# Kernel optimization log

Hardware: AMD Instinct MI355X
Metric: run time of the kernel (lower is better)

Reference implementation:

```python
import jax, jax.numpy as jnp
import numpy as np

N_NODES = 50000
N_EDGES = 800000
IN_DIM, H1, H2 = 512, 128, 64


def setup_inputs() -> dict:
    key = jax.random.key(0)
    k1, k2, k3, k4 = jax.random.split(key, 4)
    x = jax.random.normal(k1, (N_NODES, IN_DIM), dtype=jnp.float32)
    edge_index = jax.random.randint(k2, (2, N_EDGES), 0, N_NODES, dtype=jnp.int64)
    # Glorot-ish scaled weights (PyG GCNConv uses glorot init)
    W1 = jax.random.normal(k3, (IN_DIM, H1), dtype=jnp.float32) * (1.0 / np.sqrt(IN_DIM))
    b1 = jnp.zeros((H1,), dtype=jnp.float32)
    W2 = jax.random.normal(k4, (H1, H2), dtype=jnp.float32) * (1.0 / np.sqrt(H1))
    b2 = jnp.zeros((H2,), dtype=jnp.float32)
    return {"x": x, "edge_index": edge_index, "W1": W1, "b1": b1, "W2": W2, "b2": b2}


def reference(x, edge_index, W1, b1, W2, b2):
    N = x.shape[0]
    # PyG GCNConv default: add self-loops + symmetric normalization
    loop = jnp.arange(N, dtype=edge_index.dtype)
    src = jnp.concatenate([edge_index[0], loop])  # message source j
    dst = jnp.concatenate([edge_index[1], loop])  # aggregation target i
    deg = jax.ops.segment_sum(jnp.ones(src.shape[0], dtype=x.dtype), dst, num_segments=N)
    dinv = jnp.where(deg > 0, jax.lax.rsqrt(deg), 0.0)
    norm = dinv[src] * dinv[dst]  # [E+N]

    def gcn_relu(h, W, b):
        h = h @ W                                   # [N, F_out]
        msg = h[src] * norm[:, None]                # gather + edge scaling
        agg = jax.ops.segment_sum(msg, dst, num_segments=N)  # scatter-add
        return jax.nn.relu(agg + b)

    h = gcn_relu(x, W1, b1)
    return gcn_relu(h, W2, b2)
```

## Files before the change

kernel.cpp:

```cpp
#include <hip/hip_runtime.h>


constexpr int IN_DIM = 512;
constexpr int HD1 = 128;
constexpr int HD2 = 64;

typedef __attribute__((ext_vector_type(8))) short bf16x8;
typedef __attribute__((ext_vector_type(8))) unsigned short u16x8;
typedef __attribute__((ext_vector_type(4))) float f32x4;
typedef unsigned int u32;

__device__ inline unsigned short f2bf(float f) {
    u32 u = __builtin_bit_cast(u32, f);
    return (unsigned short)((u + 0x7fffu + ((u >> 16) & 1u)) >> 16);
}
__device__ inline float bf_lo(u32 v) { return __builtin_bit_cast(float, v << 16); }
__device__ inline float bf_hi(u32 v) { return __builtin_bit_cast(float, v & 0xffff0000u); }

__device__ inline int elem_off(int row, int k) {
    return (row << 6) + (k ^ ((row & 7) << 3));
}
__device__ inline int elem_off128(int row, int k) {
    return (row << 7) + (k ^ ((row & 7) << 3));
}

__global__ __launch_bounds__(256) void k_prep(const int* __restrict__ dst, int E,
                                              int* __restrict__ deg,
                                              const float* __restrict__ W1,
                                              unsigned short* __restrict__ Wt,
                                              const float* __restrict__ W2,
                                              unsigned short* __restrict__ Wt2) {
    int id = blockIdx.x * 256 + threadIdx.x;
    if (id < E) atomicAdd(&deg[dst[id]], 1);
    if (id < IN_DIM * HD1) {
        int n = id >> 9, k = id & 511;
        Wt[id] = f2bf(W1[k * HD1 + n]);
    }
    if (id < HD1 * HD2) {
        int n = id >> 7, k = id & 127;
        Wt2[id] = f2bf(W2[k * HD2 + n]);
    }
}

__global__ __launch_bounds__(256) void k_dinv_bsum(const int* __restrict__ deg, int N,
                                                   float* __restrict__ dinv,
                                                   int* __restrict__ bsum) {
    __shared__ int s[256];
    int t = threadIdx.x;
    int i = blockIdx.x * 256 + t;
    int d = (i < N) ? deg[i] : 0;
    if (i < N) dinv[i] = rsqrtf((float)(d + 1));
    s[t] = d;
    __syncthreads();
    for (int st = 128; st > 0; st >>= 1) {
        if (t < st) s[t] += s[t + st];
        __syncthreads();
    }
    if (t == 0) bsum[blockIdx.x] = s[0];
}

__global__ __launch_bounds__(1024) void k_scan_bsum(int* __restrict__ bsum, int nb) {
    __shared__ int s[1024];
    int t = threadIdx.x;
    s[t] = (t < nb) ? bsum[t] : 0;
    __syncthreads();
    for (int off = 1; off < 1024; off <<= 1) {
        int v = (t >= off) ? s[t - off] : 0;
        __syncthreads();
        s[t] += v;
        __syncthreads();
    }
    if (t < nb) bsum[t] = (t == 0) ? 0 : s[t - 1];
}

__global__ __launch_bounds__(256) void k_scan_final(const int* __restrict__ deg, int N,
                                                    const int* __restrict__ bsum,
                                                    int* __restrict__ rowptr) {
    __shared__ int s[256];
    int t = threadIdx.x;
    int i = blockIdx.x * 256 + t;
    int v = (i < N) ? deg[i] : 0;
    s[t] = v;
    __syncthreads();
    for (int off = 1; off < 256; off <<= 1) {
        int u = (t >= off) ? s[t - off] : 0;
        __syncthreads();
        s[t] += u;
        __syncthreads();
    }
    int incl = s[t] + bsum[blockIdx.x];
    if (i < N) rowptr[i] = incl - v;
    if (i == N - 1) rowptr[N] = incl;
}

__global__ __launch_bounds__(256) void k_fill(const int* __restrict__ src,
                                              const int* __restrict__ dst, int E,
                                              const int* __restrict__ rowptr,
                                              const float* __restrict__ dinv,
                                              int* __restrict__ fill,
                                              int* __restrict__ col,
                                              float* __restrict__ wgt) {
    int e = blockIdx.x * 256 + threadIdx.x;
    if (e < E) {
        int s = src[e], d = dst[e];
        int pos = rowptr[d] + atomicAdd(&fill[d], 1);
        col[pos] = s;
        wgt[pos] = dinv[s] * dinv[d];
    }
}

__global__ __launch_bounds__(256) void k_gemm1(const float* __restrict__ X,
                                               const unsigned short* __restrict__ Wt,
                                               unsigned short* __restrict__ H, int N) {
    __shared__ unsigned short As[128 * 64];
    __shared__ unsigned short Bs[128 * 64];

    const int tid = threadIdx.x;
    const int lane = tid & 63;
    const int wid = tid >> 6;
    const int brow = blockIdx.x * 128;
    const int wr0 = (wid >> 1) * 64;
    const int wc0 = (wid & 1) * 64;
    const bool full = (brow + 128 <= N);

    f32x4 acc[4][4];
#pragma unroll
    for (int i = 0; i < 4; i++)
#pragma unroll
        for (int j = 0; j < 4; j++) acc[i][j] = (f32x4){0.f, 0.f, 0.f, 0.f};

    for (int kt = 0; kt < IN_DIM / 64; kt++) {
        const int k0 = kt * 64;
#pragma unroll
        for (int p = 0; p < 4; p++) {
            int chunk = (wid * 4 + p) * 64 + lane;
            int n = chunk >> 3;
            int kcs = chunk & 7;
            int kc = kcs ^ (n & 7);
            const unsigned short* src = &Wt[(size_t)n * IN_DIM + k0 + kc * 8];
            unsigned short* dst = &Bs[(wid * 4 + p) * 512];
            __builtin_amdgcn_global_load_lds(
                (const __attribute__((address_space(1))) u32*)(const void*)src,
                (__attribute__((address_space(3))) u32*)(void*)dst, 16, 0, 0);
        }
#pragma unroll
        for (int p = 0; p < 4; p++) {
            int chunk = tid + p * 256;
            int r = chunk >> 3;
            int kc = chunk & 7;
            const float* xp = &X[(size_t)(brow + r) * IN_DIM + k0 + kc * 8];
            float4 v0, v1;
            if (full || (brow + r) < N) {
                v0 = *(const float4*)xp;
                v1 = *(const float4*)(xp + 4);
            } else {
                v0 = make_float4(0.f, 0.f, 0.f, 0.f); v1 = v0;
            }
            u16x8 w;
            w[0] = f2bf(v0.x); w[1] = f2bf(v0.y); w[2] = f2bf(v0.z); w[3] = f2bf(v0.w);
            w[4] = f2bf(v1.x); w[5] = f2bf(v1.y); w[6] = f2bf(v1.z); w[7] = f2bf(v1.w);
            *(u16x8*)&As[elem_off(r, kc * 8)] = w;
        }
        __syncthreads();

#pragma unroll
        for (int kk = 0; kk < 2; kk++) {
            const int kel = kk * 32 + (lane >> 4) * 8;
            bf16x8 a[4], b[4];
#pragma unroll
            for (int mi = 0; mi < 4; mi++)
                a[mi] = *(const bf16x8*)&As[elem_off(wr0 + mi * 16 + (lane & 15), kel)];
#pragma unroll
            for (int ni = 0; ni < 4; ni++)
                b[ni] = *(const bf16x8*)&Bs[elem_off(wc0 + ni * 16 + (lane & 15), kel)];
#pragma unroll
            for (int mi = 0; mi < 4; mi++)
#pragma unroll
                for (int ni = 0; ni < 4; ni++)
                    acc[mi][ni] = __builtin_amdgcn_mfma_f32_16x16x32_bf16(
                        a[mi], b[ni], acc[mi][ni], 0, 0, 0);
        }
        __syncthreads();
    }

#pragma unroll
    for (int mi = 0; mi < 4; mi++) {
#pragma unroll
        for (int reg = 0; reg < 4; reg++) {
            int grow = brow + wr0 + mi * 16 + (lane >> 4) * 4 + reg;
            if (grow < N) {
#pragma unroll
                for (int ni = 0; ni < 4; ni++) {
                    int gcol = wc0 + ni * 16 + (lane & 15);
                    H[(size_t)grow * HD1 + gcol] = f2bf(acc[mi][ni][reg]);
                }
            }
        }
    }
}

__global__ __launch_bounds__(256) void k_gather1(const unsigned short* __restrict__ h,
                                                 const int* __restrict__ rowptr,
                                                 const int* __restrict__ col,
                                                 const float* __restrict__ wgt,
                                                 const float* __restrict__ dinv,
                                                 const float* __restrict__ bias,
                                                 unsigned short* __restrict__ out, int N) {
    const int i = (blockIdx.x * 256 + threadIdx.x) >> 6;
    const int lane = threadIdx.x & 63;
    if (i >= N) return;
    const int half = lane >> 5;
    const int c4 = (lane & 31) * 4;
    const float di = dinv[i];
    const unsigned short* hc = h + c4;

    float a0 = 0.f, a1 = 0.f, a2 = 0.f, a3 = 0.f;
    if (half == 0) {
        uint2 sv = *(const uint2*)&hc[(size_t)i * HD1];
        float s = di * di;
        a0 = bf_lo(sv.x) * s; a1 = bf_hi(sv.x) * s;
        a2 = bf_lo(sv.y) * s; a3 = bf_hi(sv.y) * s;
    }
    const int beg = rowptr[i], end = rowptr[i + 1];
    for (int p0 = beg; p0 < end; p0 += 64) {
        int idx = p0 + lane;
        bool okl = idx < end;
        int myj = okl ? col[idx] : i;
        float myw = okl ? wgt[idx] : 0.f;
        const int cnt8 = (min(64, end - p0) + 7) & ~7;
        uint2 v[4]; float wv[4];
#pragma unroll
        for (int q = 0; q < 4; q++) {
            int e = 2 * q + half;
            int j = __shfl(myj, e);
            wv[q] = __shfl(myw, e);
            v[q] = *(const uint2*)&hc[(size_t)j * HD1];
        }
        for (int k = 8; k < cnt8; k += 8) {
            uint2 nv[4]; float nw[4];
#pragma unroll
            for (int q = 0; q < 4; q++) {
                int e = k + 2 * q + half;
                int j = __shfl(myj, e);
                nw[q] = __shfl(myw, e);
                nv[q] = *(const uint2*)&hc[(size_t)j * HD1];
            }
#pragma unroll
            for (int q = 0; q < 4; q++) {
                a0 = fmaf(bf_lo(v[q].x), wv[q], a0);
                a1 = fmaf(bf_hi(v[q].x), wv[q], a1);
                a2 = fmaf(bf_lo(v[q].y), wv[q], a2);
                a3 = fmaf(bf_hi(v[q].y), wv[q], a3);
            }
#pragma unroll
            for (int q = 0; q < 4; q++) { v[q] = nv[q]; wv[q] = nw[q]; }
        }
#pragma unroll
        for (int q = 0; q < 4; q++) {
            a0 = fmaf(bf_lo(v[q].x), wv[q], a0);
            a1 = fmaf(bf_hi(v[q].x), wv[q], a1);
            a2 = fmaf(bf_lo(v[q].y), wv[q], a2);
            a3 = fmaf(bf_hi(v[q].y), wv[q], a3);
        }
    }
    a0 += __shfl_xor(a0, 32);
    a1 += __shfl_xor(a1, 32);
    a2 += __shfl_xor(a2, 32);
    a3 += __shfl_xor(a3, 32);
    if (half == 0) {
        float4 bv = *(const float4*)&bias[c4];
        u32 w0 = (u32)f2bf(fmaxf(a0 + bv.x, 0.f)) | ((u32)f2bf(fmaxf(a1 + bv.y, 0.f)) << 16);
        u32 w1 = (u32)f2bf(fmaxf(a2 + bv.z, 0.f)) | ((u32)f2bf(fmaxf(a3 + bv.w, 0.f)) << 16);
        *(uint2*)&out[(size_t)i * HD1 + c4] = make_uint2(w0, w1);
    }
}

__global__ __launch_bounds__(256) void k_gemm2(const unsigned short* __restrict__ A,
                                               const unsigned short* __restrict__ Wt2,
                                               unsigned short* __restrict__ H, int N) {
    __shared__ unsigned short As[128 * 128];
    __shared__ unsigned short Bs[64 * 128];
    const int tid = threadIdx.x;
    const int lane = tid & 63;
    const int wid = tid >> 6;
    const int brow = blockIdx.x * 128;
    const int wr0 = wid * 32;

#pragma unroll
    for (int p = 0; p < 8; p++) {
        int chunk = (wid * 8 + p) * 64 + lane;
        int r = chunk >> 4;
        int kcs = chunk & 15;
        int kc = kcs ^ (r & 7);
        const unsigned short* src = &A[(size_t)(brow + r) * HD1 + kc * 8];
        unsigned short* dst = &As[(wid * 8 + p) * 512];
        __builtin_amdgcn_global_load_lds(
            (const __attribute__((address_space(1))) u32*)(const void*)src,
            (__attribute__((address_space(3))) u32*)(void*)dst, 16, 0, 0);
    }
#pragma unroll
    for (int p = 0; p < 4; p++) {
        int chunk = (wid * 4 + p) * 64 + lane;
        int c = chunk >> 4;
        int kcs = chunk & 15;
        int kc = kcs ^ (c & 7);
        const unsigned short* src = &Wt2[(size_t)c * HD1 + kc * 8];
        unsigned short* dst = &Bs[(wid * 4 + p) * 512];
        __builtin_amdgcn_global_load_lds(
            (const __attribute__((address_space(1))) u32*)(const void*)src,
            (__attribute__((address_space(3))) u32*)(void*)dst, 16, 0, 0);
    }
    __syncthreads();

    f32x4 acc[2][4];
#pragma unroll
    for (int i = 0; i < 2; i++)
#pragma unroll
        for (int j = 0; j < 4; j++) acc[i][j] = (f32x4){0.f, 0.f, 0.f, 0.f};

#pragma unroll
    for (int kk = 0; kk < 4; kk++) {
        const int kel = kk * 32 + (lane >> 4) * 8;
        bf16x8 a[2], b[4];
#pragma unroll
        for (int mi = 0; mi < 2; mi++)
            a[mi] = *(const bf16x8*)&As[elem_off128(wr0 + mi * 16 + (lane & 15), kel)];
#pragma unroll
        for (int ni = 0; ni < 4; ni++)
            b[ni] = *(const bf16x8*)&Bs[elem_off128(ni * 16 + (lane & 15), kel)];
#pragma unroll
        for (int mi = 0; mi < 2; mi++)
#pragma unroll
            for (int ni = 0; ni < 4; ni++)
                acc[mi][ni] = __builtin_amdgcn_mfma_f32_16x16x32_bf16(
                    a[mi], b[ni], acc[mi][ni], 0, 0, 0);
    }

#pragma unroll
    for (int mi = 0; mi < 2; mi++) {
#pragma unroll
        for (int reg = 0; reg < 4; reg++) {
            int grow = brow + wr0 + mi * 16 + (lane >> 4) * 4 + reg;
            if (grow < N) {
#pragma unroll
                for (int ni = 0; ni < 4; ni++) {
                    int gcol = ni * 16 + (lane & 15);
                    H[(size_t)grow * HD2 + gcol] = f2bf(acc[mi][ni][reg]);
                }
            }
        }
    }
}

__global__ __launch_bounds__(256) void k_gather2(const unsigned short* __restrict__ h,
                                                 const int* __restrict__ rowptr,
                                                 const int* __restrict__ col,
                                                 const float* __restrict__ wgt,
                                                 const float* __restrict__ dinv,
                                                 const float* __restrict__ bias,
                                                 float* __restrict__ out, int N) {
    const int i = (blockIdx.x * 256 + threadIdx.x) >> 6;
    const int lane = threadIdx.x & 63;
    if (i >= N) return;
    const int half = lane >> 5;
    const int c2 = (lane & 31) * 2;
    const float di = dinv[i];
    const unsigned short* hc = h + c2;

    float a0 = 0.f, a1 = 0.f;
    if (half == 0) {
        u32 sv = *(const u32*)&hc[(size_t)i * HD2];
        float s = di * di;
        a0 = bf_lo(sv) * s; a1 = bf_hi(sv) * s;
    }
    const int beg = rowptr[i], end = rowptr[i + 1];
    for (int p0 = beg; p0 < end; p0 += 64) {
        int idx = p0 + lane;
        bool okl = idx < end;
        int myj = okl ? col[idx] : i;
        float myw = okl ? wgt[idx] : 0.f;
        const int cnt8 = (min(64, end - p0) + 7) & ~7;
        u32 v[4]; float wv[4];
#pragma unroll
        for (int q = 0; q < 4; q++) {
            int e = 2 * q + half;
            int j = __shfl(myj, e);
            wv[q] = __shfl(myw, e);
            v[q] = *(const u32*)&hc[(size_t)j * HD2];
        }
        for (int k = 8; k < cnt8; k += 8) {
            u32 nv[4]; float nw[4];
#pragma unroll
            for (int q = 0; q < 4; q++) {
                int e = k + 2 * q + half;
                int j = __shfl(myj, e);
                nw[q] = __shfl(myw, e);
                nv[q] = *(const u32*)&hc[(size_t)j * HD2];
            }
#pragma unroll
            for (int q = 0; q < 4; q++) {
                a0 = fmaf(bf_lo(v[q]), wv[q], a0);
                a1 = fmaf(bf_hi(v[q]), wv[q], a1);
            }
#pragma unroll
            for (int q = 0; q < 4; q++) { v[q] = nv[q]; wv[q] = nw[q]; }
        }
#pragma unroll
        for (int q = 0; q < 4; q++) {
            a0 = fmaf(bf_lo(v[q]), wv[q], a0);
            a1 = fmaf(bf_hi(v[q]), wv[q], a1);
        }
    }
    a0 += __shfl_xor(a0, 32);
    a1 += __shfl_xor(a1, 32);
    if (half == 0) {
        float2 bv = *(const float2*)&bias[c2];
        float2 r = make_float2(fmaxf(a0 + bv.x, 0.f), fmaxf(a1 + bv.y, 0.f));
        *(float2*)&out[(size_t)i * HD2 + c2] = r;
    }
}

extern "C" void kernel_launch(void* const* d_in, const int* in_sizes, int n_in,
                              void* d_out, int out_size, void* d_ws, size_t ws_size,
                              hipStream_t stream) {
    const float* x  = (const float*)d_in[0];
    const int*   ei = (const int*)d_in[1];
    const float* W1 = (const float*)d_in[2];
    const float* b1 = (const float*)d_in[3];
    const float* W2 = (const float*)d_in[4];
    const float* b2 = (const float*)d_in[5];
    float* out = (float*)d_out;

    const int N = in_sizes[0] / IN_DIM;
    const int E = in_sizes[1] / 2;
    const int* src = ei;
    const int* dst = ei + E;

    char* w = (char*)d_ws;
    size_t off = 0;
    auto alloc = [&](size_t bytes) -> void* {
        void* p = w + off;
        off = (off + bytes + 255) & ~(size_t)255;
        return p;
    };
    int*   deg    = (int*)alloc((size_t)N * 4);
    int*   fill   = (int*)alloc((size_t)N * 4);
    int*   rowptr = (int*)alloc((size_t)(N + 1) * 4);
    int*   bsum   = (int*)alloc(1024 * 4);
    int*   col    = (int*)alloc((size_t)E * 4);
    float* wgt    = (float*)alloc((size_t)E * 4);
    float* dinv   = (float*)alloc((size_t)N * 4);
    unsigned short* Wt  = (unsigned short*)alloc((size_t)IN_DIM * HD1 * 2);
    unsigned short* Wt2 = (unsigned short*)alloc((size_t)HD2 * HD1 * 2);
    unsigned short* h1  = (unsigned short*)alloc((size_t)N * HD1 * 2);
    unsigned short* agg1= (unsigned short*)alloc((size_t)(N + 128) * HD1 * 2);
    unsigned short* h2  = h1;

    size_t zero_span = (size_t)((char*)fill - (char*)deg) + (size_t)N * 4;
    hipMemsetAsync(deg, 0, zero_span, stream);

    const int nb = (N + 255) / 256;
    const int eb = (E + 255) / 256;

    k_prep<<<eb, 256, 0, stream>>>(dst, E, deg, W1, Wt, W2, Wt2);
    k_dinv_bsum<<<nb, 256, 0, stream>>>(deg, N, dinv, bsum);
    k_scan_bsum<<<1, 1024, 0, stream>>>(bsum, nb);
    k_scan_final<<<nb, 256, 0, stream>>>(deg, N, bsum, rowptr);
    k_fill<<<eb, 256, 0, stream>>>(src, dst, E, rowptr, dinv, fill, col, wgt);

    k_gemm1<<<(N + 127) / 128, 256, 0, stream>>>(x, Wt, h1, N);
    k_gather1<<<(N * 64 + 255) / 256, 256, 0, stream>>>(h1, rowptr, col, wgt, dinv, b1, agg1, N);
    k_gemm2<<<(N + 127) / 128, 256, 0, stream>>>(agg1, Wt2, h2, N);
    k_gather2<<<(N * 64 + 255) / 256, 256, 0, stream>>>(h2, rowptr, col, wgt, dinv, b2, out, N);
}
```

Before: 179.4 us.

## Co-schedule CSR fill with GEMM1 in one launch; compute edge weights on the fly

Merges the CSR fill kernel and the first GEMM into one launch. Extra blocks past the GEMM tiles run a grid-stride edge fill, so the memory/atomic-bound fill overlaps the compute-bound GEMM. The per-edge weight array is dropped: the gather kernels load dinv[col] per edge and multiply by the destination's dinv, which saves a 3.2MB write and re-read but adds a dependent random load per edge chunk. Fill blocks compete with GEMM blocks for CUs and LDS, since the unused shared arrays are still allocated.

```diff
diff --git a/kernel.cpp b/kernel.cpp
--- a/kernel.cpp
+++ b/kernel.cpp
@@ -93,27 +93,27 @@
     if (i == N - 1) rowptr[N] = incl;
 }
 
-__global__ __launch_bounds__(256) void k_fill(const int* __restrict__ src,
+__global__ __launch_bounds__(256) void k_mega(const float* __restrict__ X,
+                                              const unsigned short* __restrict__ Wt,
+                                              unsigned short* __restrict__ H, int N,
+                                              int gemmBlocks,
+                                              const int* __restrict__ src,
                                               const int* __restrict__ dst, int E,
                                               const int* __restrict__ rowptr,
-                                              const float* __restrict__ dinv,
                                               int* __restrict__ fill,
-                                              int* __restrict__ col,
-                                              float* __restrict__ wgt) {
-    int e = blockIdx.x * 256 + threadIdx.x;
-    if (e < E) {
-        int s = src[e], d = dst[e];
-        int pos = rowptr[d] + atomicAdd(&fill[d], 1);
-        col[pos] = s;
-        wgt[pos] = dinv[s] * dinv[d];
-    }
-}
-
-__global__ __launch_bounds__(256) void k_gemm1(const float* __restrict__ X,
-                                               const unsigned short* __restrict__ Wt,
-                                               unsigned short* __restrict__ H, int N) {
+                                              int* __restrict__ col) {
     __shared__ unsigned short As[128 * 64];
     __shared__ unsigned short Bs[128 * 64];
+
+    if (blockIdx.x >= gemmBlocks) {
+        int stride = (gridDim.x - gemmBlocks) * 256;
+        for (int e = (blockIdx.x - gemmBlocks) * 256 + threadIdx.x; e < E; e += stride) {
+            int s = src[e], d = dst[e];
+            int pos = rowptr[d] + atomicAdd(&fill[d], 1);
+            col[pos] = s;
+        }
+        return;
+    }
 
     const int tid = threadIdx.x;
     const int lane = tid & 63;
@@ -137,11 +137,11 @@
             int n = chunk >> 3;
             int kcs = chunk & 7;
             int kc = kcs ^ (n & 7);
-            const unsigned short* src = &Wt[(size_t)n * IN_DIM + k0 + kc * 8];
-            unsigned short* dst = &Bs[(wid * 4 + p) * 512];
+            const unsigned short* srcp = &Wt[(size_t)n * IN_DIM + k0 + kc * 8];
+            unsigned short* dstp = &Bs[(wid * 4 + p) * 512];
             __builtin_amdgcn_global_load_lds(
-                (const __attribute__((address_space(1))) u32*)(const void*)src,
-                (__attribute__((address_space(3))) u32*)(void*)dst, 16, 0, 0);
+                (const __attribute__((address_space(1))) u32*)(const void*)srcp,
+                (__attribute__((address_space(3))) u32*)(void*)dstp, 16, 0, 0);
         }
 #pragma unroll
         for (int p = 0; p < 4; p++) {
@@ -202,7 +202,6 @@
 __global__ __launch_bounds__(256) void k_gather1(const unsigned short* __restrict__ h,
                                                  const int* __restrict__ rowptr,
                                                  const int* __restrict__ col,
-                                                 const float* __restrict__ wgt,
                                                  const float* __restrict__ dinv,
                                                  const float* __restrict__ bias,
                                                  unsigned short* __restrict__ out, int N) {
@@ -226,14 +225,14 @@
         int idx = p0 + lane;
         bool okl = idx < end;
         int myj = okl ? col[idx] : i;
-        float myw = okl ? wgt[idx] : 0.f;
+        float mydj = okl ? dinv[myj] : 0.f;
         const int cnt8 = (min(64, end - p0) + 7) & ~7;
         uint2 v[4]; float wv[4];
 #pragma unroll
         for (int q = 0; q < 4; q++) {
             int e = 2 * q + half;
             int j = __shfl(myj, e);
-            wv[q] = __shfl(myw, e);
+            wv[q] = __shfl(mydj, e) * di;
             v[q] = *(const uint2*)&hc[(size_t)j * HD1];
         }
         for (int k = 8; k < cnt8; k += 8) {
@@ -242,7 +241,7 @@
             for (int q = 0; q < 4; q++) {
                 int e = k + 2 * q + half;
                 int j = __shfl(myj, e);
-                nw[q] = __shfl(myw, e);
+                nw[q] = __shfl(mydj, e) * di;
                 nv[q] = *(const uint2*)&hc[(size_t)j * HD1];
             }
 #pragma unroll
@@ -355,7 +354,6 @@
 __global__ __launch_bounds__(256) void k_gather2(const unsigned short* __restrict__ h,
                                                  const int* __restrict__ rowptr,
                                                  const int* __restrict__ col,
-                                                 const float* __restrict__ wgt,
                                                  const float* __restrict__ dinv,
                                                  const float* __restrict__ bias,
                                                  float* __restrict__ out, int N) {
@@ -378,14 +376,14 @@
         int idx = p0 + lane;
         bool okl = idx < end;
         int myj = okl ? col[idx] : i;
-        float myw = okl ? wgt[idx] : 0.f;
+        float mydj = okl ? dinv[myj] : 0.f;
         const int cnt8 = (min(64, end - p0) + 7) & ~7;
         u32 v[4]; float wv[4];
 #pragma unroll
         for (int q = 0; q < 4; q++) {
             int e = 2 * q + half;
             int j = __shfl(myj, e);
-            wv[q] = __shfl(myw, e);
+            wv[q] = __shfl(mydj, e) * di;
             v[q] = *(const u32*)&hc[(size_t)j * HD2];
         }
         for (int k = 8; k < cnt8; k += 8) {
@@ -394,7 +392,7 @@
             for (int q = 0; q < 4; q++) {
                 int e = k + 2 * q + half;
                 int j = __shfl(myj, e);
-                nw[q] = __shfl(myw, e);
+                nw[q] = __shfl(mydj, e) * di;
                 nv[q] = *(const u32*)&hc[(size_t)j * HD2];
             }
 #pragma unroll
@@ -448,7 +446,6 @@
     int*   rowptr = (int*)alloc((size_t)(N + 1) * 4);
     int*   bsum   = (int*)alloc(1024 * 4);
     int*   col    = (int*)alloc((size_t)E * 4);
-    float* wgt    = (float*)alloc((size_t)E * 4);
     float* dinv   = (float*)alloc((size_t)N * 4);
     unsigned short* Wt  = (unsigned short*)alloc((size_t)IN_DIM * HD1 * 2);
     unsigned short* Wt2 = (unsigned short*)alloc((size_t)HD2 * HD1 * 2);
@@ -461,15 +458,18 @@
 
     const int nb = (N + 255) / 256;
     const int eb = (E + 255) / 256;
+    const int gemmBlocks = (N + 127) / 128;
+    const int fillBlocks = 512;
 
     k_prep<<<eb, 256, 0, stream>>>(dst, E, deg, W1, Wt, W2, Wt2);
     k_dinv_bsum<<<nb, 256, 0, stream>>>(deg, N, dinv, bsum);
     k_scan_bsum<<<1, 1024, 0, stream>>>(bsum, nb);
     k_scan_final<<<nb, 256, 0, stream>>>(deg, N, bsum, rowptr);
-    k_fill<<<eb, 256, 0, stream>>>(src, dst, E, rowptr, dinv, fill, col, wgt);
-
-    k_gemm1<<<(N + 127) / 128, 256, 0, stream>>>(x, Wt, h1, N);
-    k_gather1<<<(N * 64 + 255) / 256, 256, 0, stream>>>(h1, rowptr, col, wgt, dinv, b1, agg1, N);
+
+    k_mega<<<gemmBlocks + fillBlocks, 256, 0, stream>>>(
+        x, Wt, h1, N, gemmBlocks, src, dst, E, rowptr, fill, col);
+
+    k_gather1<<<(N * 64 + 255) / 256, 256, 0, stream>>>(h1, rowptr, col, dinv, b1, agg1, N);
     k_gemm2<<<(N + 127) / 128, 256, 0, stream>>>(agg1, Wt2, h2, N);
-    k_gather2<<<(N * 64 + 255) / 256, 256, 0, stream>>>(h2, rowptr, col, wgt, dinv, b2, out, N);
-}
+    k_gather2<<<(N * 64 + 255) / 256, 256, 0, stream>>>(h2, rowptr, col, dinv, b2, out, N);
+}
```

New measurement: 169.2 us. 5.7% less time.
